# Kernel tuning notes

Hardware: AMD Instinct MI355X
Metric: run time of the kernel (lower is better)

The kernel has to match this reference:

```python
import jax, jax.numpy as jnp
import numpy as np

B, T, D = 4, 2048, 768
H = 12
DH = D // H
DFF = 3072
EPS = 1e-5


def _layernorm(x, g, b):
    mu = jnp.mean(x, axis=-1, keepdims=True)
    var = jnp.var(x, axis=-1, keepdims=True)
    return (x - mu) * jax.lax.rsqrt(var + EPS) * g + b


def setup_inputs() -> dict:
    key = jax.random.key(0)
    ks = jax.random.split(key, 12)
    s = lambda fan_in: 1.0 / np.sqrt(fan_in)
    return {
        "x": jax.random.normal(ks[0], (B, T, D), dtype=jnp.float32),
        "ln1_g": jnp.ones((D,), jnp.float32),
        "ln1_b": jnp.zeros((D,), jnp.float32),
        "w_qkv": jax.random.uniform(ks[1], (D, 3 * D), jnp.float32, -s(D), s(D)),
        "b_qkv": jax.random.uniform(ks[2], (3 * D,), jnp.float32, -s(D), s(D)),
        "w_proj": jax.random.uniform(ks[3], (D, D), jnp.float32, -s(D), s(D)),
        "b_proj": jax.random.uniform(ks[4], (D,), jnp.float32, -s(D), s(D)),
        "ln2_g": jnp.ones((D,), jnp.float32),
        "ln2_b": jnp.zeros((D,), jnp.float32),
        "w_ff1": jax.random.uniform(ks[5], (D, DFF), jnp.float32, -s(D), s(D)),
        "b_ff1": jax.random.uniform(ks[6], (DFF,), jnp.float32, -s(D), s(D)),
        "w_ff2": jax.random.uniform(ks[7], (DFF, D), jnp.float32, -s(DFF), s(DFF)),
        "b_ff2": jax.random.uniform(ks[8], (D,), jnp.float32, -s(DFF), s(DFF)),
    }


def reference(x, ln1_g, ln1_b, w_qkv, b_qkv, w_proj, b_proj,
              ln2_g, ln2_b, w_ff1, b_ff1, w_ff2, b_ff2):
    # --- attention sublayer ---
    h = _layernorm(x, ln1_g, ln1_b)
    qkv = h @ w_qkv + b_qkv                       # [B,T,3D]
    q, k, v = jnp.split(qkv, 3, axis=-1)
    q = q.reshape(B, T, H, DH).transpose(0, 2, 1, 3)  # [B,H,T,DH]
    k = k.reshape(B, T, H, DH).transpose(0, 2, 1, 3)
    v = v.reshape(B, T, H, DH).transpose(0, 2, 1, 3)
    att = jnp.einsum('bhqd,bhkd->bhqk', q, k) / jnp.sqrt(jnp.float32(DH))
    causal = jnp.tril(jnp.ones((T, T), dtype=bool))
    att = jnp.where(causal, att, -jnp.inf)
    att = jax.nn.softmax(att, axis=-1)
    out = jnp.einsum('bhqk,bhkd->bhqd', att, v)    # [B,H,T,DH]
    out = out.transpose(0, 2, 1, 3).reshape(B, T, D)
    x = x + out @ w_proj + b_proj
    # --- MLP sublayer ---
    h2 = _layernorm(x, ln2_g, ln2_b)
    h2 = jax.nn.gelu(h2 @ w_ff1 + b_ff1, approximate=False)
    x = x + h2 @ w_ff2 + b_ff2
    return x
```

## Files before the change

kernel.cpp:

```cpp
#include <hip/hip_runtime.h>
#include <cstdint>
#include <cstddef>

typedef unsigned short u16;
typedef unsigned int u32;
typedef __attribute__((ext_vector_type(8))) short s16x8;
typedef __attribute__((ext_vector_type(4))) float f32x4;

#define NB 4
#define NT 2048
#define ND 768
#define NH 12
#define NDH 64
#define NFF 3072
#define NM (NB*NT)

__device__ __forceinline__ u16 f2b(float f){
  union { float f; unsigned u; } c; c.f = f;
  unsigned r = c.u + 0x7fffu + ((c.u >> 16) & 1u);
  return (u16)(r >> 16);
}

__device__ __forceinline__ f32x4 mfma16(s16x8 a, s16x8 b, f32x4 c){
  return __builtin_amdgcn_mfma_f32_16x16x32_bf16(a, b, c, 0, 0, 0);
}

__device__ __forceinline__ void stage16(u16* lds, const u16* g){
  __builtin_amdgcn_global_load_lds(
      (const __attribute__((address_space(1))) unsigned int*)g,
      (__attribute__((address_space(3))) unsigned int*)lds,
      16, 0, 0);
}

__device__ __forceinline__ float gelu_f(float v){
  const float x = v * 0.70710678118654752f;
  const float ax = fabsf(x);
  const float t = 1.f / (1.f + 0.3275911f * ax);
  const float y = t * (0.254829592f + t * (-0.284496736f + t * (1.421413741f
                + t * (-1.453152027f + t * 1.061405429f))));
  float er = 1.f - y * __expf(-ax * ax);
  er = copysignf(er, x);
  return 0.5f * v * (1.f + er);
}

__global__ __launch_bounds__(256) void transpose_all(
    const float* __restrict__ w_qkv, const float* __restrict__ w_proj,
    const float* __restrict__ w_ff1, const float* __restrict__ w_ff2,
    u16* __restrict__ o_qkv, u16* __restrict__ o_proj,
    u16* __restrict__ o_ff1, u16* __restrict__ o_ff2)
{
  int bid = blockIdx.x;
  const float* in; u16* out; int K, N, nx;
  if (bid < 1728)      { in = w_qkv;  out = o_qkv;  K = 768;  N = 2304; nx = 72; }
  else if ((bid -= 1728) < 576)  { in = w_proj; out = o_proj; K = 768;  N = 768;  nx = 24; }
  else if ((bid -= 576) < 2304)  { in = w_ff1;  out = o_ff1;  K = 768;  N = 3072; nx = 96; }
  else { bid -= 2304;              in = w_ff2;  out = o_ff2;  K = 3072; N = 768;  nx = 24; }
  const int n0 = (bid % nx) * 32, k0 = (bid / nx) * 32;

  __shared__ float tile[32][33];
  const int tx = threadIdx.x, ty = threadIdx.y;
  #pragma unroll
  for (int i = 0; i < 32; i += 8)
    tile[ty + i][tx] = in[(size_t)(k0 + ty + i) * N + n0 + tx];
  __syncthreads();
  #pragma unroll
  for (int i = 0; i < 32; i += 8)
    out[(size_t)(n0 + ty + i) * K + k0 + tx] = f2b(tile[tx][ty + i]);
}

__global__ __launch_bounds__(256) void ln_kernel(
    const float* __restrict__ x, const float* __restrict__ g,
    const float* __restrict__ b, u16* __restrict__ out)
{
  const int row = blockIdx.x;
  const int t = threadIdx.x;
  const float* xr = x + (size_t)row * ND;
  float v0 = xr[t], v1 = xr[t + 256], v2 = xr[t + 512];
  float s = v0 + v1 + v2;
  float ss = v0*v0 + v1*v1 + v2*v2;
  #pragma unroll
  for (int o = 32; o; o >>= 1) { s += __shfl_xor(s, o, 64); ss += __shfl_xor(ss, o, 64); }
  __shared__ float red[8];
  const int w = t >> 6;
  if ((t & 63) == 0) { red[w] = s; red[4 + w] = ss; }
  __syncthreads();
  s  = red[0] + red[1] + red[2] + red[3];
  ss = red[4] + red[5] + red[6] + red[7];
  const float mu = s * (1.f / ND);
  const float var = ss * (1.f / ND) - mu * mu;
  const float rinv = rsqrtf(var + 1e-5f);
  u16* orow = out + (size_t)row * ND;
  orow[t]       = f2b((v0 - mu) * rinv * g[t]       + b[t]);
  orow[t + 256] = f2b((v1 - mu) * rinv * g[t + 256] + b[t + 256]);
  orow[t + 512] = f2b((v2 - mu) * rinv * g[t + 512] + b[t + 512]);
}

template<int EPI, int BM>
__global__ __launch_bounds__(256, (BM == 128) ? 3 : 4) void gemm_bt(
    const u16* __restrict__ A, const u16* __restrict__ Bt,
    const float* __restrict__ bias, const float* __restrict__ res,
    void* __restrict__ o0, void* __restrict__ o1, void* __restrict__ o2,
    const int M, const int N, const int K)
{
  constexpr int MI = BM / 64;
  __shared__ u16 As[3][BM * 32];
  __shared__ u16 Bs[3][128 * 32];
  const int tid = threadIdx.x;
  const int lane = tid & 63, wid = tid >> 6;
  const int wr = wid >> 1, wc = wid & 1;
  const int lg = lane >> 4, lm = lane & 15;
  const int bm = blockIdx.x * BM, bn = blockIdx.y * 128;

  f32x4 acc[2 * MI][4] = {};

  const int srow = tid >> 2;
  const int schunk = (tid & 3) ^ ((tid >> 3) & 3);
  const u16* ApT = A  + (size_t)(bm + srow) * K + schunk * 8;
  const u16* BpT = Bt + (size_t)(bn + srow) * K + schunk * 8;
  const size_t rs64 = (size_t)64 * K;
  const int woff = wid * 512;
  const int fswz = (lm >> 1) & 3;

  const int nt = K >> 5;

  #pragma unroll
  for (int p = 0; p < 2; ++p) {
    const int k0 = p << 5;
    stage16(&As[p][woff], ApT + k0);
    if (BM == 128) stage16(&As[p][woff + 2048], ApT + rs64 + k0);
    stage16(&Bs[p][woff],        BpT + k0);
    stage16(&Bs[p][woff + 2048], BpT + rs64 + k0);
  }

  for (int t = 0; t < nt; ++t) {
    if (t < nt - 1) {
      if (BM == 128) asm volatile("s_waitcnt vmcnt(4)" ::: "memory");
      else           asm volatile("s_waitcnt vmcnt(3)" ::: "memory");
    } else {
      asm volatile("s_waitcnt vmcnt(0)" ::: "memory");
    }
    __builtin_amdgcn_s_barrier();
    __builtin_amdgcn_sched_barrier(0);
    if (t + 2 < nt) {
      const int k0 = (t + 2) << 5;
      const int wb = (t + 2) % 3;
      stage16(&As[wb][woff], ApT + k0);
      if (BM == 128) stage16(&As[wb][woff + 2048], ApT + rs64 + k0);
      stage16(&Bs[wb][woff],        BpT + k0);
      stage16(&Bs[wb][woff + 2048], BpT + rs64 + k0);
    }
    __builtin_amdgcn_sched_barrier(0);
    const int rb = t % 3;
    s16x8 af[2 * MI], bf[4];
    #pragma unroll
    for (int i = 0; i < 2 * MI; i++)
      af[i] = *(const s16x8*)&As[rb][(wr * (BM / 2) + i * 16 + lm) * 32 + ((lg ^ fswz) * 8)];
    #pragma unroll
    for (int j = 0; j < 4; j++)
      bf[j] = *(const s16x8*)&Bs[rb][(wc * 64 + j * 16 + lm) * 32 + ((lg ^ fswz) * 8)];
    #pragma unroll
    for (int i = 0; i < 2 * MI; i++)
      #pragma unroll
      for (int j = 0; j < 4; j++)
        acc[i][j] = mfma16(af[i], bf[j], acc[i][j]);
  }

  #pragma unroll
  for (int i = 0; i < 2 * MI; i++)
    #pragma unroll
    for (int j = 0; j < 4; j++) {
      const int col = bn + wc * 64 + j * 16 + lm;
      const float bb = bias[col];
      #pragma unroll
      for (int r = 0; r < 4; r++) {
        const int row = bm + wr * (BM / 2) + i * 16 + lg * 4 + r;
        float v = acc[i][j][r] + bb;
        if (EPI == 0) {
          u16* dst; int rem;
          if (col < ND)            { dst = (u16*)o0; rem = col; v *= 0.125f; }
          else if (col < 2 * ND)   { dst = (u16*)o1; rem = col - ND; }
          else                     { dst = (u16*)o2; rem = col - 2 * ND; }
          const int hh = rem >> 6, dh = rem & 63;
          const int bb2 = row >> 11, tt = row & 2047;
          dst[(((size_t)bb2 * NH + hh) * NT + tt) * NDH + dh] = f2b(v);
        } else if (EPI == 1) {
          ((float*)o0)[(size_t)row * ND + col] = v + res[(size_t)row * ND + col];
        } else if (EPI == 2) {
          ((u16*)o0)[(size_t)row * NFF + col] = f2b(gelu_f(v));
        } else {
          ((float*)o0)[(size_t)row * ND + col] = v + res[(size_t)row * ND + col];
        }
      }
    }
}

__global__ __launch_bounds__(256,2) void attn_kernel(
    const u16* __restrict__ Q, const u16* __restrict__ Kg,
    const u16* __restrict__ V, u16* __restrict__ O)
{
  const int pairIdx = blockIdx.y;
  const int bh = blockIdx.x;
  const int b = bh / NH, h = bh % NH;
  const int tid = threadIdx.x;
  const int lane = tid & 63, w = tid >> 6;
  const int lg = lane >> 4, lm = lane & 15;
  const int sr = tid >> 3;
  const int sc = (tid & 7) * 8;

  __shared__ u16 Ks[64 * 64];
  __shared__ u16 Vt[64 * 64];
  __shared__ u16 Ps[4][16 * 64];

  const u16* Qb = Q  + (size_t)bh * NT * NDH;
  const u16* Kb = Kg + (size_t)bh * NT * NDH;
  const u16* Vb = V  + (size_t)bh * NT * NDH;

  for (int half = 0; half < 2; ++half) {
    const int si = half ? (31 - pairIdx) : pairIdx;
    const int q0 = si * 64;
    const int ktmax = si;

    const s16x8 qf0 = *(const s16x8*)&Qb[(size_t)(q0 + w * 16 + lm) * NDH + lg * 8];
    const s16x8 qf1 = *(const s16x8*)&Qb[(size_t)(q0 + w * 16 + lm) * NDH + 32 + lg * 8];

    f32x4 oacc[4] = {};
    float m = -INFINITY, l = 0.f;

    s16x8 kva = *(const s16x8*)&Kb[(size_t)sr * NDH + sc];
    s16x8 kvb = *(const s16x8*)&Kb[(size_t)(sr + 32) * NDH + sc];
    s16x8 vva = *(const s16x8*)&Vb[(size_t)sr * NDH + sc];
    s16x8 vvb = *(const s16x8*)&Vb[(size_t)(sr + 32) * NDH + sc];

    for (int kt = 0; kt <= ktmax; ++kt) {
      __syncthreads();
      *(s16x8*)&Ks[sr * 64 + (sc ^ ((sr & 7) << 3))] = kva;
      *(s16x8*)&Ks[(sr + 32) * 64 + (sc ^ ((sr & 7) << 3))] = kvb;
      #pragma unroll
      for (int e = 0; e < 8; ++e)
        Vt[(sc + e) * 64 + (sr ^ ((((tid & 7) ^ e)) << 3))] = (u16)vva[e];
      #pragma unroll
      for (int e = 0; e < 8; ++e)
        Vt[(sc + e) * 64 + ((sr + 32) ^ ((((tid & 7) ^ e)) << 3))] = (u16)vvb[e];
      __syncthreads();

      if (kt < ktmax) {
        const u16* Kn = Kb + (size_t)(kt + 1) * 64 * NDH;
        const u16* Vn = Vb + (size_t)(kt + 1) * 64 * NDH;
        kva = *(const s16x8*)&Kn[(size_t)sr * NDH + sc];
        kvb = *(const s16x8*)&Kn[(size_t)(sr + 32) * NDH + sc];
        vva = *(const s16x8*)&Vn[(size_t)sr * NDH + sc];
        vvb = *(const s16x8*)&Vn[(size_t)(sr + 32) * NDH + sc];
      }

      f32x4 sv[4];
      #pragma unroll
      for (int n = 0; n < 4; ++n) {
        const int krow = (n * 16 + lm) * 64;
        const int swz = (lm & 7) << 3;
        s16x8 kf0 = *(const s16x8*)&Ks[krow + ((lg * 8) ^ swz)];
        s16x8 kf1 = *(const s16x8*)&Ks[krow + ((32 + lg * 8) ^ swz)];
        f32x4 s4 = {};
        s4 = mfma16(kf0, qf0, s4);
        s4 = mfma16(kf1, qf1, s4);
        sv[n] = s4;
      }

      if (kt == ktmax) {
        #pragma unroll
        for (int n = 0; n < 4; ++n)
          #pragma unroll
          for (int r = 0; r < 4; ++r)
            if (n * 16 + lg * 4 + r > w * 16 + lm) sv[n][r] = -INFINITY;
      }

      float mx = -INFINITY;
      #pragma unroll
      for (int n = 0; n < 4; ++n)
        #pragma unroll
        for (int r = 0; r < 4; ++r) mx = fmaxf(mx, sv[n][r]);
      mx = fmaxf(mx, __shfl_xor(mx, 16));
      mx = fmaxf(mx, __shfl_xor(mx, 32));
      const float mnew = fmaxf(m, mx);
      const float alpha = __expf(m - mnew);
      m = mnew;

      float rs = 0.f;
      u32 pk[4][2];
      #pragma unroll
      for (int n = 0; n < 4; ++n) {
        const float p0 = __expf(sv[n][0] - mnew);
        const float p1 = __expf(sv[n][1] - mnew);
        const float p2 = __expf(sv[n][2] - mnew);
        const float p3 = __expf(sv[n][3] - mnew);
        rs += (p0 + p1) + (p2 + p3);
        pk[n][0] = (u32)f2b(p0) | ((u32)f2b(p1) << 16);
        pk[n][1] = (u32)f2b(p2) | ((u32)f2b(p3) << 16);
      }
      rs += __shfl_xor(rs, 16);
      rs += __shfl_xor(rs, 32);
      l = l * alpha + rs;

      #pragma unroll
      for (int n = 0; n < 4; ++n) {
        const int idx0 = lm * 64 + ((n * 16 + lg * 4) ^ ((lm & 7) << 3));
        *(u32*)&Ps[w][idx0] = pk[n][0];
        *(u32*)&Ps[w][idx0 + 2] = pk[n][1];
      }

      float av[4];
      #pragma unroll
      for (int r = 0; r < 4; ++r) av[r] = __shfl(alpha, lg * 4 + r);
      #pragma unroll
      for (int d = 0; d < 4; ++d)
        #pragma unroll
        for (int r = 0; r < 4; ++r) oacc[d][r] *= av[r];

      #pragma unroll
      for (int kh = 0; kh < 2; ++kh) {
        const s16x8 pf = *(const s16x8*)&Ps[w][lm * 64 + ((kh * 32 + lg * 8) ^ ((lm & 7) << 3))];
        #pragma unroll
        for (int dt = 0; dt < 4; ++dt) {
          const int g = ((2 * dt + (lm >> 3)) ^ (lm & 7)) & 7;
          const s16x8 vf = *(const s16x8*)&Vt[(dt * 16 + lm) * 64 + (((kh * 4 + lg) ^ g) << 3)];
          oacc[dt] = mfma16(pf, vf, oacc[dt]);
        }
      }
    }

    float lv[4];
    #pragma unroll
    for (int r = 0; r < 4; ++r) lv[r] = 1.f / __shfl(l, lg * 4 + r);
    #pragma unroll
    for (int dt = 0; dt < 4; ++dt)
      #pragma unroll
      for (int r = 0; r < 4; ++r) {
        const int qg = q0 + w * 16 + lg * 4 + r;
        O[((size_t)b * NT + qg) * ND + h * NDH + dt * 16 + lm] = f2b(oacc[dt][r] * lv[r]);
      }
  }
}

extern "C" void kernel_launch(void* const* d_in, const int* in_sizes, int n_in,
                              void* d_out, int out_size, void* d_ws, size_t ws_size,
                              hipStream_t stream)
{
  const float* x      = (const float*)d_in[0];
  const float* ln1_g  = (const float*)d_in[1];
  const float* ln1_b  = (const float*)d_in[2];
  const float* w_qkv  = (const float*)d_in[3];
  const float* b_qkv  = (const float*)d_in[4];
  const float* w_proj = (const float*)d_in[5];
  const float* b_proj = (const float*)d_in[6];
  const float* ln2_g  = (const float*)d_in[7];
  const float* ln2_b  = (const float*)d_in[8];
  const float* w_ff1  = (const float*)d_in[9];
  const float* b_ff1  = (const float*)d_in[10];
  const float* w_ff2  = (const float*)d_in[11];
  const float* b_ff2  = (const float*)d_in[12];

  char* ws = (char*)d_ws;
  u16*   wt_qkv = (u16*)(ws + 0);
  u16*   wt_proj= (u16*)(ws + 3538944);
  u16*   wt_ff1 = (u16*)(ws + 4718592);
  u16*   wt_ff2 = (u16*)(ws + 9437184);
  u16*   hbuf   = (u16*)(ws + 14155776);
  u16*   qbuf   = (u16*)(ws + 26738688);
  u16*   kbuf   = (u16*)(ws + 39321600);
  u16*   vbuf   = (u16*)(ws + 51904512);
  u16*   aobuf  = (u16*)(ws + 64487424);
  float* x1     = (float*)(ws + 77070336);
  u16*   h2buf  = (u16*)(ws + 102236160);
  u16*   ff1buf = hbuf;

  transpose_all<<<6912, dim3(32,8), 0, stream>>>(w_qkv, w_proj, w_ff1, w_ff2,
                                                 wt_qkv, wt_proj, wt_ff1, wt_ff2);

  ln_kernel<<<NM, 256, 0, stream>>>(x, ln1_g, ln1_b, hbuf);
  gemm_bt<0,128><<<dim3(NM/128, 2304/128), 256, 0, stream>>>(hbuf, wt_qkv, b_qkv, nullptr,
                                                             qbuf, kbuf, vbuf, NM, 2304, ND);
  attn_kernel<<<dim3(NB*NH, 16), 256, 0, stream>>>(qbuf, kbuf, vbuf, aobuf);
  gemm_bt<1,64><<<dim3(NM/64, ND/128), 256, 0, stream>>>(aobuf, wt_proj, b_proj, x,
                                                         x1, nullptr, nullptr, NM, ND, ND);
  ln_kernel<<<NM, 256, 0, stream>>>(x1, ln2_g, ln2_b, h2buf);
  gemm_bt<2,128><<<dim3(NM/128, NFF/128), 256, 0, stream>>>(h2buf, wt_ff1, b_ff1, nullptr,
                                                            ff1buf, nullptr, nullptr, NM, NFF, ND);
  gemm_bt<3,64><<<dim3(NM/64, ND/128), 256, 0, stream>>>(ff1buf, wt_ff2, b_ff2, x1,
                                                         d_out, nullptr, nullptr, NM, ND, NFF);
}
```

Baseline: 289.6 us.

## Process paired causal query strips in one pass sharing K/V tiles

The attention kernel used to process its two query strips (p and 31-p) one after the other, loading K/V tiles from global memory separately for each. It now walks the K/V tiles once up to the later strip's diagonal and updates both strips' online-softmax accumulators from the same shared-memory tile. This removes roughly a third of the K/V global loads, LDS staging and barriers for each block. The cost is a second set of output accumulators and Q fragments held in registers, which raises register pressure and may reduce occupancy.

```diff
diff --git a/kernel.cpp b/kernel.cpp
--- a/kernel.cpp
+++ b/kernel.cpp
@@ -198,7 +198,7 @@
     const u16* __restrict__ Q, const u16* __restrict__ Kg,
     const u16* __restrict__ V, u16* __restrict__ O)
 {
-  const int pairIdx = blockIdx.y;
+  const int p  = blockIdx.y;
   const int bh = blockIdx.x;
   const int b = bh / NH, h = bh % NH;
   const int tid = threadIdx.x;
@@ -215,127 +215,145 @@
   const u16* Kb = Kg + (size_t)bh * NT * NDH;
   const u16* Vb = V  + (size_t)bh * NT * NDH;
 
-  for (int half = 0; half < 2; ++half) {
-    const int si = half ? (31 - pairIdx) : pairIdx;
-    const int q0 = si * 64;
-    const int ktmax = si;
-
-    const s16x8 qf0 = *(const s16x8*)&Qb[(size_t)(q0 + w * 16 + lm) * NDH + lg * 8];
-    const s16x8 qf1 = *(const s16x8*)&Qb[(size_t)(q0 + w * 16 + lm) * NDH + 32 + lg * 8];
-
-    f32x4 oacc[4] = {};
-    float m = -INFINITY, l = 0.f;
-
-    s16x8 kva = *(const s16x8*)&Kb[(size_t)sr * NDH + sc];
-    s16x8 kvb = *(const s16x8*)&Kb[(size_t)(sr + 32) * NDH + sc];
-    s16x8 vva = *(const s16x8*)&Vb[(size_t)sr * NDH + sc];
-    s16x8 vvb = *(const s16x8*)&Vb[(size_t)(sr + 32) * NDH + sc];
-
-    for (int kt = 0; kt <= ktmax; ++kt) {
-      __syncthreads();
-      *(s16x8*)&Ks[sr * 64 + (sc ^ ((sr & 7) << 3))] = kva;
-      *(s16x8*)&Ks[(sr + 32) * 64 + (sc ^ ((sr & 7) << 3))] = kvb;
-      #pragma unroll
-      for (int e = 0; e < 8; ++e)
-        Vt[(sc + e) * 64 + (sr ^ ((((tid & 7) ^ e)) << 3))] = (u16)vva[e];
-      #pragma unroll
-      for (int e = 0; e < 8; ++e)
-        Vt[(sc + e) * 64 + ((sr + 32) ^ ((((tid & 7) ^ e)) << 3))] = (u16)vvb[e];
-      __syncthreads();
-
-      if (kt < ktmax) {
-        const u16* Kn = Kb + (size_t)(kt + 1) * 64 * NDH;
-        const u16* Vn = Vb + (size_t)(kt + 1) * 64 * NDH;
-        kva = *(const s16x8*)&Kn[(size_t)sr * NDH + sc];
-        kvb = *(const s16x8*)&Kn[(size_t)(sr + 32) * NDH + sc];
-        vva = *(const s16x8*)&Vn[(size_t)sr * NDH + sc];
-        vvb = *(const s16x8*)&Vn[(size_t)(sr + 32) * NDH + sc];
-      }
-
-      f32x4 sv[4];
-      #pragma unroll
-      for (int n = 0; n < 4; ++n) {
-        const int krow = (n * 16 + lm) * 64;
-        const int swz = (lm & 7) << 3;
-        s16x8 kf0 = *(const s16x8*)&Ks[krow + ((lg * 8) ^ swz)];
-        s16x8 kf1 = *(const s16x8*)&Ks[krow + ((32 + lg * 8) ^ swz)];
-        f32x4 s4 = {};
-        s4 = mfma16(kf0, qf0, s4);
-        s4 = mfma16(kf1, qf1, s4);
-        sv[n] = s4;
-      }
-
-      if (kt == ktmax) {
-        #pragma unroll
-        for (int n = 0; n < 4; ++n)
-          #pragma unroll
-          for (int r = 0; r < 4; ++r)
-            if (n * 16 + lg * 4 + r > w * 16 + lm) sv[n][r] = -INFINITY;
-      }
-
-      float mx = -INFINITY;
+  const int si0 = p, si1 = 31 - p;
+  const int q00 = si0 * 64, q01 = si1 * 64;
+  const int ktmax = si1;
+
+  const s16x8 q0a = *(const s16x8*)&Qb[(size_t)(q00 + w * 16 + lm) * NDH + lg * 8];
+  const s16x8 q0b = *(const s16x8*)&Qb[(size_t)(q00 + w * 16 + lm) * NDH + 32 + lg * 8];
+  const s16x8 q1a = *(const s16x8*)&Qb[(size_t)(q01 + w * 16 + lm) * NDH + lg * 8];
+  const s16x8 q1b = *(const s16x8*)&Qb[(size_t)(q01 + w * 16 + lm) * NDH + 32 + lg * 8];
+
+  f32x4 oacc0[4] = {}, oacc1[4] = {};
+  float m0 = -INFINITY, l0 = 0.f, m1 = -INFINITY, l1 = 0.f;
+
+  auto do_strip = [&](const s16x8& qa, const s16x8& qb, f32x4* oacc,
+                      float& m, float& l, bool diag) {
+    f32x4 sv[4];
+    #pragma unroll
+    for (int n = 0; n < 4; ++n) {
+      const int krow = (n * 16 + lm) * 64;
+      const int swz = (lm & 7) << 3;
+      s16x8 kf0 = *(const s16x8*)&Ks[krow + ((lg * 8) ^ swz)];
+      s16x8 kf1 = *(const s16x8*)&Ks[krow + ((32 + lg * 8) ^ swz)];
+      f32x4 s4 = {};
+      s4 = mfma16(kf0, qa, s4);
+      s4 = mfma16(kf1, qb, s4);
+      sv[n] = s4;
+    }
+    if (diag) {
       #pragma unroll
       for (int n = 0; n < 4; ++n)
         #pragma unroll
-        for (int r = 0; r < 4; ++r) mx = fmaxf(mx, sv[n][r]);
-      mx = fmaxf(mx, __shfl_xor(mx, 16));
-      mx = fmaxf(mx, __shfl_xor(mx, 32));
-      const float mnew = fmaxf(m, mx);
-      const float alpha = __expf(m - mnew);
-      m = mnew;
-
-      float rs = 0.f;
-      u32 pk[4][2];
-      #pragma unroll
-      for (int n = 0; n < 4; ++n) {
-        const float p0 = __expf(sv[n][0] - mnew);
-        const float p1 = __expf(sv[n][1] - mnew);
-        const float p2 = __expf(sv[n][2] - mnew);
-        const float p3 = __expf(sv[n][3] - mnew);
-        rs += (p0 + p1) + (p2 + p3);
-        pk[n][0] = (u32)f2b(p0) | ((u32)f2b(p1) << 16);
-        pk[n][1] = (u32)f2b(p2) | ((u32)f2b(p3) << 16);
+        for (int r = 0; r < 4; ++r)
+          if (n * 16 + lg * 4 + r > w * 16 + lm) sv[n][r] = -INFINITY;
+    }
+    float mx = -INFINITY;
+    #pragma unroll
+    for (int n = 0; n < 4; ++n)
+      #pragma unroll
+      for (int r = 0; r < 4; ++r) mx = fmaxf(mx, sv[n][r]);
+    mx = fmaxf(mx, __shfl_xor(mx, 16));
+    mx = fmaxf(mx, __shfl_xor(mx, 32));
+    const float mnew = fmaxf(m, mx);
+    const float alpha = __expf(m - mnew);
+    m = mnew;
+
+    float rs = 0.f;
+    u32 pk[4][2];
+    #pragma unroll
+    for (int n = 0; n < 4; ++n) {
+      const float p0 = __expf(sv[n][0] - mnew);
+      const float p1 = __expf(sv[n][1] - mnew);
+      const float p2 = __expf(sv[n][2] - mnew);
+      const float p3 = __expf(sv[n][3] - mnew);
+      rs += (p0 + p1) + (p2 + p3);
+      pk[n][0] = (u32)f2b(p0) | ((u32)f2b(p1) << 16);
+      pk[n][1] = (u32)f2b(p2) | ((u32)f2b(p3) << 16);
+    }
+    rs += __shfl_xor(rs, 16);
+    rs += __shfl_xor(rs, 32);
+    l = l * alpha + rs;
+
+    #pragma unroll
+    for (int n = 0; n < 4; ++n) {
+      const int idx0 = lm * 64 + ((n * 16 + lg * 4) ^ ((lm & 7) << 3));
+      *(u32*)&Ps[w][idx0] = pk[n][0];
+      *(u32*)&Ps[w][idx0 + 2] = pk[n][1];
+    }
+
+    float av[4];
+    #pragma unroll
+    for (int r = 0; r < 4; ++r) av[r] = __shfl(alpha, lg * 4 + r);
+    #pragma unroll
+    for (int d = 0; d < 4; ++d)
+      #pragma unroll
+      for (int r = 0; r < 4; ++r) oacc[d][r] *= av[r];
+
+    #pragma unroll
+    for (int kh = 0; kh < 2; ++kh) {
+      const s16x8 pf = *(const s16x8*)&Ps[w][lm * 64 + ((kh * 32 + lg * 8) ^ ((lm & 7) << 3))];
+      #pragma unroll
+      for (int dt = 0; dt < 4; ++dt) {
+        const int g = ((2 * dt + (lm >> 3)) ^ (lm & 7)) & 7;
+        const s16x8 vf = *(const s16x8*)&Vt[(dt * 16 + lm) * 64 + (((kh * 4 + lg) ^ g) << 3)];
+        oacc[dt] = mfma16(pf, vf, oacc[dt]);
       }
-      rs += __shfl_xor(rs, 16);
-      rs += __shfl_xor(rs, 32);
-      l = l * alpha + rs;
-
-      #pragma unroll
-      for (int n = 0; n < 4; ++n) {
-        const int idx0 = lm * 64 + ((n * 16 + lg * 4) ^ ((lm & 7) << 3));
-        *(u32*)&Ps[w][idx0] = pk[n][0];
-        *(u32*)&Ps[w][idx0 + 2] = pk[n][1];
+    }
+  };
+
+  s16x8 kva = *(const s16x8*)&Kb[(size_t)sr * NDH + sc];
+  s16x8 kvb = *(const s16x8*)&Kb[(size_t)(sr + 32) * NDH + sc];
+  s16x8 vva = *(const s16x8*)&Vb[(size_t)sr * NDH + sc];
+  s16x8 vvb = *(const s16x8*)&Vb[(size_t)(sr + 32) * NDH + sc];
+
+  for (int kt = 0; kt <= ktmax; ++kt) {
+    __syncthreads();
+    *(s16x8*)&Ks[sr * 64 + (sc ^ ((sr & 7) << 3))] = kva;
+    *(s16x8*)&Ks[(sr + 32) * 64 + (sc ^ ((sr & 7) << 3))] = kvb;
+    #pragma unroll
+    for (int e = 0; e < 8; ++e)
+      Vt[(sc + e) * 64 + (sr ^ ((((tid & 7) ^ e)) << 3))] = (u16)vva[e];
+    #pragma unroll
+    for (int e = 0; e < 8; ++e)
+      Vt[(sc + e) * 64 + ((sr + 32) ^ ((((tid & 7) ^ e)) << 3))] = (u16)vvb[e];
+    __syncthreads();
+
+    if (kt < ktmax) {
+      const u16* Kn = Kb + (size_t)(kt + 1) * 64 * NDH;
+      const u16* Vn = Vb + (size_t)(kt + 1) * 64 * NDH;
+      kva = *(const s16x8*)&Kn[(size_t)sr * NDH + sc];
+      kvb = *(const s16x8*)&Kn[(size_t)(sr + 32) * NDH + sc];
+      vva = *(const s16x8*)&Vn[(size_t)sr * NDH + sc];
+      vvb = *(const s16x8*)&Vn[(size_t)(sr + 32) * NDH + sc];
+    }
+
+    do_strip(q1a, q1b, oacc1, m1, l1, kt == si1);
+    if (kt <= si0) do_strip(q0a, q0b, oacc0, m0, l0, kt == si0);
+  }
+
+  {
+    float lv[4];
+    #pragma unroll
+    for (int r = 0; r < 4; ++r) lv[r] = 1.f / __shfl(l0, lg * 4 + r);
+    #pragma unroll
+    for (int dt = 0; dt < 4; ++dt)
+      #pragma unroll
+      for (int r = 0; r < 4; ++r) {
+        const int qg = q00 + w * 16 + lg * 4 + r;
+        O[((size_t)b * NT + qg) * ND + h * NDH + dt * 16 + lm] = f2b(oacc0[dt][r] * lv[r]);
       }
-
-      float av[4];
-      #pragma unroll
-      for (int r = 0; r < 4; ++r) av[r] = __shfl(alpha, lg * 4 + r);
-      #pragma unroll
-      for (int d = 0; d < 4; ++d)
-        #pragma unroll
-        for (int r = 0; r < 4; ++r) oacc[d][r] *= av[r];
-
-      #pragma unroll
-      for (int kh = 0; kh < 2; ++kh) {
-        const s16x8 pf = *(const s16x8*)&Ps[w][lm * 64 + ((kh * 32 + lg * 8) ^ ((lm & 7) << 3))];
-        #pragma unroll
-        for (int dt = 0; dt < 4; ++dt) {
-          const int g = ((2 * dt + (lm >> 3)) ^ (lm & 7)) & 7;
-          const s16x8 vf = *(const s16x8*)&Vt[(dt * 16 + lm) * 64 + (((kh * 4 + lg) ^ g) << 3)];
-          oacc[dt] = mfma16(pf, vf, oacc[dt]);
-        }
-      }
-    }
-
+  }
+  {
     float lv[4];
     #pragma unroll
-    for (int r = 0; r < 4; ++r) lv[r] = 1.f / __shfl(l, lg * 4 + r);
+    for (int r = 0; r < 4; ++r) lv[r] = 1.f / __shfl(l1, lg * 4 + r);
     #pragma unroll
     for (int dt = 0; dt < 4; ++dt)
       #pragma unroll
       for (int r = 0; r < 4; ++r) {
-        const int qg = q0 + w * 16 + lg * 4 + r;
-        O[((size_t)b * NT + qg) * ND + h * NDH + dt * 16 + lm] = f2b(oacc[dt][r] * lv[r]);
+        const int qg = q01 + w * 16 + lg * 4 + r;
+        O[((size_t)b * NT + qg) * ND + h * NDH + dt * 16 + lm] = f2b(oacc1[dt][r] * lv[r]);
       }
   }
 }
```

Result: faster. 281.8 us, median of 3 (-2.7%).
